# Optimization experiments

Hardware: AMD Instinct MI355X
Metric: run time of the kernel (lower is better)

Reference implementation:

```python
import jax, jax.numpy as jnp
import numpy as np

E, D, H, T = 16, 1024, 4096, 8192  # num_expert, d_model, d_hidden (4h), total tokens


def setup_inputs() -> dict:
    key = jax.random.key(0)
    k0, k1, k2, k3, k4 = jax.random.split(key, 5)
    inp = jax.random.normal(k0, (T, D), dtype=jnp.float32)
    # FMoELinear init: kaiming-uniform-like, bound = 1/sqrt(fan_in)
    s1 = 1.0 / np.sqrt(D)
    s2 = 1.0 / np.sqrt(H)
    w1 = jax.random.uniform(k1, (E, H, D), jnp.float32, -s1, s1)  # htoh4 weight [E, out, in]
    b1 = jax.random.uniform(k2, (E, H), jnp.float32, -s1, s1)
    w2 = jax.random.uniform(k3, (E, D, H), jnp.float32, -s2, s2)  # h4toh weight
    b2 = jax.random.uniform(k4, (E, D), jnp.float32, -s2, s2)
    fwd_expert_count = jnp.full((E,), T // E, dtype=jnp.int32)  # tokens per expert (sums to T)
    return dict(inp=inp, w1=w1, b1=b1, w2=w2, b2=b2, fwd_expert_count=fwd_expert_count)


def reference(inp, w1, b1, w2, b2, fwd_expert_count):
    # Grouped GEMM: tokens are sorted by expert; segment e gets expert e's FFN.
    counts = np.asarray(fwd_expert_count)          # static per-expert row counts
    offs = np.concatenate([[0], np.cumsum(counts)])
    outs = []
    for e in range(counts.shape[0]):               # loop over fixed small expert set
        seg = inp[offs[e]:offs[e + 1]]             # [n_e, D]
        h = seg @ w1[e].T + b1[e]                  # htoh4: [n_e, H]
        h = jax.nn.gelu(h, approximate=False)      # torch F.gelu default (exact)
        outs.append(h @ w2[e].T + b2[e])           # h4toh: [n_e, D]
    return jnp.concatenate(outs, axis=0)           # [T, D]
```

## Files before the change

### kernel.cpp

```cpp
#include <hip/hip_runtime.h>
#include <hip/hip_bf16.h>

typedef float f32x4 __attribute__((ext_vector_type(4)));
typedef int   i32x4 __attribute__((ext_vector_type(4)));
typedef __bf16 bf16x8 __attribute__((ext_vector_type(8)));
typedef unsigned short u16;
typedef unsigned short u16x4 __attribute__((ext_vector_type(4)));
typedef unsigned short u16x8 __attribute__((ext_vector_type(8)));

#define BM 128
#define BN 128
#define BK 32
#define NT 256
#define MAXE 32

__device__ __forceinline__ u16 f2bf(float f) {
  __bf16 h = (__bf16)f;
  return __builtin_bit_cast(u16, h);
}

__global__ __launch_bounds__(256)
void cvt_bf16(const float* __restrict__ in, u16* __restrict__ out, int n8) {
  int i = blockIdx.x * 256 + threadIdx.x;
  if (i < n8) {
    f32x4 a = *(const f32x4*)(in + (long long)i * 8);
    f32x4 b = *(const f32x4*)(in + (long long)i * 8 + 4);
    u16x8 r = { f2bf(a[0]), f2bf(a[1]), f2bf(a[2]), f2bf(a[3]),
                f2bf(b[0]), f2bf(b[1]), f2bf(b[2]), f2bf(b[3]) };
    *(u16x8*)(out + (long long)i * 8) = r;
  }
}

template<bool DO_GELU, bool OUT_BF16, int NTB>
__global__ __launch_bounds__(NT)
void ffn_gemm(const u16* __restrict__ Ain, const float* __restrict__ Bw,
              const float* __restrict__ bias, void* __restrict__ Out,
              const int* __restrict__ counts, int E, int T, int N, int K)
{
  int cs[MAXE];
#pragma unroll
  for (int j = 0; j < MAXE / 4; ++j) {
    if (j * 4 + 3 < E) {
      *(i32x4*)&cs[j * 4] = *(const i32x4*)(counts + j * 4);
    } else {
#pragma unroll
      for (int q = 0; q < 4; ++q) cs[j*4+q] = (j*4+q < E) ? counts[j*4+q] : 0;
    }
  }
  int mt = blockIdx.y, row0 = 0, e = -1, cnt = 0;
#pragma unroll
  for (int i = 0; i < MAXE; ++i) {
    if (i < E && e < 0) {
      int ntl = (cs[i] + BM - 1) / BM;
      if (mt < ntl) { e = i; cnt = cs[i]; }
      else { mt -= ntl; row0 += cs[i]; }
    }
  }
  if (e < 0) return;
  int valid = cnt - mt * BM; if (valid > BM) valid = BM;
  row0 += mt * BM;

  const float* Be = Bw + (long long)e * N * K;
  const float* be = bias + (long long)e * N;

  __shared__ u16 As[2][BM][BK];
  __shared__ u16 Bs[2][BN][BK];

  const int t = threadIdx.x;
  const int lane = t & 63;
  const int w = t >> 6, wr = w >> 1, wc = w & 1;
  const int NKT = K / BK;

  long long offA[2];
#pragma unroll
  for (int i = 0; i < 2; ++i) {
    int c = i * NT + t;
    int row = c >> 2, col = (c & 3) << 3;
    int gr = row0 + row; if (gr > T - 1) gr = T - 1;
    offA[i] = (long long)gr * K + col;
  }
  int rBrow[4], rBcol[4];
#pragma unroll
  for (int i = 0; i < 4; ++i) {
    int c = i * NT + t;
    rBrow[i] = c >> 3; rBcol[i] = (c & 7) << 2;
  }

  const int rl = lane & 15;
  const int kgf = (lane >> 4) ^ ((rl >> 1) & 3);
  const int cl = lane & 15, rg = lane >> 4;

  u16x8 rAu[2]; float rB[16];

  for (int pass = 0; pass < NTB; ++pass) {
    const int n0 = (blockIdx.x * NTB + pass) * BN;

    long long offB[4];
#pragma unroll
    for (int i = 0; i < 4; ++i)
      offB[i] = (long long)(n0 + rBrow[i]) * K + rBcol[i];

    f32x4 acc[4][4];
#pragma unroll
    for (int i = 0; i < 4; ++i)
#pragma unroll
      for (int j = 0; j < 4; ++j) acc[i][j] = (f32x4){0.f, 0.f, 0.f, 0.f};

    auto load_g = [&](int kt) {
      const int k0 = kt * BK;
#pragma unroll
      for (int i = 0; i < 2; ++i)
        rAu[i] = *(const u16x8*)(Ain + offA[i] + k0);
#pragma unroll
      for (int i = 0; i < 4; ++i) {
        f32x4 v = *(const f32x4*)(Be + offB[i] + k0);
        rB[i*4+0] = v[0]; rB[i*4+1] = v[1]; rB[i*4+2] = v[2]; rB[i*4+3] = v[3];
      }
    };

    auto store_tile = [&](int buf) {
#pragma unroll
      for (int i = 0; i < 2; ++i) {
        int c = i * NT + t;
        int row = c >> 2, col = (c & 3) << 3;
        int kg = (col >> 3) ^ ((row >> 1) & 3);
        *(u16x8*)&As[buf][row][kg * 8] = rAu[i];
      }
#pragma unroll
      for (int i = 0; i < 4; ++i) {
        int c = i * NT + t;
        int row = c >> 3, col = (c & 7) << 2;
        int kg = (col >> 3) ^ ((row >> 1) & 3);
        int off = kg * 8 + ((col >> 2) & 1) * 4;
        u16x4 pk = { f2bf(rB[i*4+0]), f2bf(rB[i*4+1]), f2bf(rB[i*4+2]), f2bf(rB[i*4+3]) };
        *(u16x4*)&Bs[buf][row][off] = pk;
      }
    };

    if (NTB > 1 && pass > 0) __syncthreads();

    load_g(0);
    store_tile(0);
    load_g(1);
    __syncthreads();

    for (int kt = 0; kt < NKT; ++kt) {
      const int cur = kt & 1;

      bf16x8 af[4], bfr[4];
#pragma unroll
      for (int mf = 0; mf < 4; ++mf)
        af[mf] = __builtin_bit_cast(bf16x8, *(const u16x8*)&As[cur][wr*64 + mf*16 + rl][kgf*8]);
#pragma unroll
      for (int nf = 0; nf < 4; ++nf)
        bfr[nf] = __builtin_bit_cast(bf16x8, *(const u16x8*)&Bs[cur][wc*64 + nf*16 + rl][kgf*8]);

      if (kt + 1 < NKT) store_tile(cur ^ 1);
      if (kt + 2 < NKT) load_g(kt + 2);

#pragma unroll
      for (int mf = 0; mf < 4; ++mf)
#pragma unroll
        for (int nf = 0; nf < 4; ++nf)
          acc[mf][nf] = __builtin_amdgcn_mfma_f32_16x16x32_bf16(af[mf], bfr[nf], acc[mf][nf], 0, 0, 0);

      if (kt + 1 < NKT) __syncthreads();
    }

#pragma unroll
    for (int mf = 0; mf < 4; ++mf) {
#pragma unroll
      for (int nf = 0; nf < 4; ++nf) {
        int gcol = n0 + wc*64 + nf*16 + cl;
        float bv = be[gcol];
#pragma unroll
        for (int r = 0; r < 4; ++r) {
          int lrow = wr*64 + mf*16 + rg*4 + r;
          if (lrow < valid) {
            float v = acc[mf][nf][r] + bv;
            if constexpr (DO_GELU)
              v = 0.5f * v * (1.0f + erff(v * 0.70710678118654752f));
            long long idx = (long long)(row0 + lrow) * N + gcol;
            if constexpr (OUT_BF16) ((u16*)Out)[idx] = f2bf(v);
            else                    ((float*)Out)[idx] = v;
          }
        }
      }
    }
  }
}

extern "C" void kernel_launch(void* const* d_in, const int* in_sizes, int n_in,
                              void* d_out, int out_size, void* d_ws, size_t ws_size,
                              hipStream_t stream) {
  const float* inp = (const float*)d_in[0];
  const float* w1  = (const float*)d_in[1];
  const float* b1  = (const float*)d_in[2];
  const float* w2  = (const float*)d_in[3];
  const float* b2  = (const float*)d_in[4];
  const int* cnts  = (const int*)d_in[5];

  const int E = in_sizes[5];
  const int H = in_sizes[2] / E;
  const int D = in_sizes[4] / E;
  const int T = in_sizes[0] / D;

  u16* hbuf = (u16*)d_ws;
  u16* ibuf = (u16*)((char*)d_ws + (size_t)T * H * 2);

  const int n8 = (T * D) / 8;
  cvt_bf16<<<dim3((n8 + 255) / 256), dim3(256), 0, stream>>>(inp, ibuf, n8);

  const int tiles = (T + BM - 1) / BM + E;

  constexpr int NTB1 = 4;
  dim3 g1(H / BN / NTB1, tiles);
  ffn_gemm<true, true, NTB1><<<g1, dim3(NT), 0, stream>>>(
      ibuf, w1, b1, (void*)hbuf, cnts, E, T, H, D);

  dim3 g2(D / BN, tiles);
  ffn_gemm<false, false, 1><<<g2, dim3(NT), 0, stream>>>(
      hbuf, w2, b2, d_out, cnts, E, T, D, H);
}
```

Before: 351.9 us.

## Use direct global-to-LDS loads with fp32 weight staging in first FFN GEMM

```diff
diff --git a/kernel.cpp b/kernel.cpp
--- a/kernel.cpp
+++ b/kernel.cpp
@@ -17,6 +17,12 @@
 __device__ __forceinline__ u16 f2bf(float f) {
   __bf16 h = (__bf16)f;
   return __builtin_bit_cast(u16, h);
+}
+
+typedef const __attribute__((address_space(1))) void GAS;
+typedef __attribute__((address_space(3))) void LAS;
+__device__ __forceinline__ void gl_lds16(const void* g, void* l) {
+  __builtin_amdgcn_global_load_lds((GAS*)g, (LAS*)l, 16, 0, 0);
 }
 
 __global__ __launch_bounds__(256)
@@ -31,34 +37,161 @@
   }
 }
 
-template<bool DO_GELU, bool OUT_BF16, int NTB>
+__device__ __forceinline__ int expert_lookup(const int* counts, int E, int bm,
+                                             int mt_in, int& row0, int& cnt, int& mt) {
+  int cs[MAXE];
+#pragma unroll
+  for (int j = 0; j < MAXE / 4; ++j) {
+    if (j * 4 + 3 < E) *(i32x4*)&cs[j * 4] = *(const i32x4*)(counts + j * 4);
+    else {
+#pragma unroll
+      for (int q = 0; q < 4; ++q) cs[j*4+q] = (j*4+q < E) ? counts[j*4+q] : 0;
+    }
+  }
+  int e = -1; row0 = 0; cnt = 0; mt = mt_in;
+#pragma unroll
+  for (int i = 0; i < MAXE; ++i) {
+    if (i < E && e < 0) {
+      int ntl = (cs[i] + bm - 1) / bm;
+      if (mt < ntl) { e = i; cnt = cs[i]; }
+      else { mt -= ntl; row0 += cs[i]; }
+    }
+  }
+  return e;
+}
+
+__global__ __launch_bounds__(NT)
+void ffn_gemm1(const u16* __restrict__ Ain, const float* __restrict__ Bw,
+               const float* __restrict__ bias, u16* __restrict__ Out,
+               const int* __restrict__ counts, int E, int T, int N, int K)
+{
+  int row0, cnt, mt;
+  int e = expert_lookup(counts, E, BM, blockIdx.y, row0, cnt, mt);
+  if (e < 0) return;
+  int valid = cnt - mt * BM; if (valid > BM) valid = BM;
+  row0 += mt * BM;
+  const int n0 = blockIdx.x * BN;
+
+  const float* Be = Bw + (long long)e * N * K;
+  const float* be = bias + (long long)e * N;
+
+  __shared__ u16  As[2][BM * BK];
+  __shared__ float Bs[2][BN * BK];
+
+  const int t = threadIdx.x;
+  const int lane = t & 63;
+  const int w = t >> 6, wr = w >> 1, wc = w & 1;
+  const int NKT = K / BK;
+
+  int aSrc[2], aDst[2];
+#pragma unroll
+  for (int s = 0; s < 2; ++s) {
+    int rb = (s * 4 + w) * 16;
+    int r = rb + (lane >> 2);
+    int gr = row0 + r; if (gr > T - 1) gr = T - 1;
+    aSrc[s] = gr * K + ((lane & 3) << 3);
+    aDst[s] = rb * BK;
+  }
+  int bSrc[4], bDst[4];
+#pragma unroll
+  for (int s = 0; s < 4; ++s) {
+    int rb = (s * 4 + w) * 8;
+    int r = rb + (lane >> 3);
+    bSrc[s] = (n0 + r) * K + (((lane & 7) ^ (r & 7)) << 2);
+    bDst[s] = rb * BK;
+  }
+
+  auto stage = [&](int buf, int kt) {
+    const int k0 = kt * BK;
+#pragma unroll
+    for (int s = 0; s < 2; ++s) gl_lds16(Ain + aSrc[s] + k0, &As[buf][aDst[s]]);
+#pragma unroll
+    for (int s = 0; s < 4; ++s) gl_lds16(Be + bSrc[s] + k0, &Bs[buf][bDst[s]]);
+  };
+
+  const int rl = lane & 15, kg = lane >> 4;
+  int aoff[4], boff[4];
+#pragma unroll
+  for (int mf = 0; mf < 4; ++mf) {
+    int R = wr * 64 + mf * 16 + rl;
+    aoff[mf] = R * BK + kg * 8;
+  }
+#pragma unroll
+  for (int nf = 0; nf < 4; ++nf) {
+    int R = wc * 64 + nf * 16 + rl;
+    int go = (2 * kg) ^ (R & 7);
+    boff[nf] = R * BK + go * 4;
+  }
+
+  f32x4 acc[4][4];
+#pragma unroll
+  for (int i = 0; i < 4; ++i)
+#pragma unroll
+    for (int j = 0; j < 4; ++j) acc[i][j] = (f32x4){0.f, 0.f, 0.f, 0.f};
+
+  stage(0, 0);
+  __syncthreads();
+
+  for (int kt = 0; kt < NKT; ++kt) {
+    const int cur = kt & 1;
+    if (kt + 1 < NKT) stage(cur ^ 1, kt + 1);
+
+    bf16x8 af[4], bfr[4];
+#pragma unroll
+    for (int mf = 0; mf < 4; ++mf)
+      af[mf] = __builtin_bit_cast(bf16x8, *(const u16x8*)&As[cur][aoff[mf]]);
+#pragma unroll
+    for (int nf = 0; nf < 4; ++nf) {
+      f32x4 lo = *(const f32x4*)&Bs[cur][boff[nf]];
+      f32x4 hi = *(const f32x4*)&Bs[cur][boff[nf] ^ 4];
+      u16x8 r = { f2bf(lo[0]), f2bf(lo[1]), f2bf(lo[2]), f2bf(lo[3]),
+                  f2bf(hi[0]), f2bf(hi[1]), f2bf(hi[2]), f2bf(hi[3]) };
+      bfr[nf] = __builtin_bit_cast(bf16x8, r);
+    }
+
+    __builtin_amdgcn_s_setprio(1);
+#pragma unroll
+    for (int mf = 0; mf < 4; ++mf)
+#pragma unroll
+      for (int nf = 0; nf < 4; ++nf)
+        acc[mf][nf] = __builtin_amdgcn_mfma_f32_16x16x32_bf16(af[mf], bfr[nf], acc[mf][nf], 0, 0, 0);
+    __builtin_amdgcn_s_setprio(0);
+
+    __syncthreads();
+  }
+
+  const int cl = lane & 15, rg = lane >> 4;
+#pragma unroll
+  for (int mf = 0; mf < 4; ++mf) {
+#pragma unroll
+    for (int nf = 0; nf < 4; ++nf) {
+      int gcol = n0 + wc * 64 + nf * 16 + cl;
+      float bv = be[gcol];
+#pragma unroll
+      for (int r = 0; r < 4; ++r) {
+        int lrow = wr * 64 + mf * 16 + rg * 4 + r;
+        if (lrow < valid) {
+          float v = acc[mf][nf][r] + bv;
+          v = 0.5f * v * (1.0f + erff(v * 0.70710678118654752f));
+          Out[(long long)(row0 + lrow) * N + gcol] = f2bf(v);
+        }
+      }
+    }
+  }
+}
+
+template<bool DO_GELU, bool OUT_BF16>
 __global__ __launch_bounds__(NT)
 void ffn_gemm(const u16* __restrict__ Ain, const float* __restrict__ Bw,
               const float* __restrict__ bias, void* __restrict__ Out,
               const int* __restrict__ counts, int E, int T, int N, int K)
 {
-  int cs[MAXE];
-#pragma unroll
-  for (int j = 0; j < MAXE / 4; ++j) {
-    if (j * 4 + 3 < E) {
-      *(i32x4*)&cs[j * 4] = *(const i32x4*)(counts + j * 4);
-    } else {
-#pragma unroll
-      for (int q = 0; q < 4; ++q) cs[j*4+q] = (j*4+q < E) ? counts[j*4+q] : 0;
-    }
-  }
-  int mt = blockIdx.y, row0 = 0, e = -1, cnt = 0;
-#pragma unroll
-  for (int i = 0; i < MAXE; ++i) {
-    if (i < E && e < 0) {
-      int ntl = (cs[i] + BM - 1) / BM;
-      if (mt < ntl) { e = i; cnt = cs[i]; }
-      else { mt -= ntl; row0 += cs[i]; }
-    }
-  }
+  int row0, cnt, mt;
+  int e = expert_lookup(counts, E, BM, blockIdx.y, row0, cnt, mt);
   if (e < 0) return;
   int valid = cnt - mt * BM; if (valid > BM) valid = BM;
   row0 += mt * BM;
+  const int n0 = blockIdx.x * BN;
 
   const float* Be = Bw + (long long)e * N * K;
   const float* be = bias + (long long)e * N;
@@ -79,111 +212,100 @@
     int gr = row0 + row; if (gr > T - 1) gr = T - 1;
     offA[i] = (long long)gr * K + col;
   }
-  int rBrow[4], rBcol[4];
+  long long offB[4];
 #pragma unroll
   for (int i = 0; i < 4; ++i) {
     int c = i * NT + t;
-    rBrow[i] = c >> 3; rBcol[i] = (c & 7) << 2;
-  }
+    offB[i] = (long long)(n0 + (c >> 3)) * K + ((c & 7) << 2);
+  }
+
+  f32x4 acc[4][4];
+#pragma unroll
+  for (int i = 0; i < 4; ++i)
+#pragma unroll
+    for (int j = 0; j < 4; ++j) acc[i][j] = (f32x4){0.f, 0.f, 0.f, 0.f};
+
+  u16x8 rAu[2]; float rB[16];
+
+  auto load_g = [&](int kt) {
+    const int k0 = kt * BK;
+#pragma unroll
+    for (int i = 0; i < 2; ++i)
+      rAu[i] = *(const u16x8*)(Ain + offA[i] + k0);
+#pragma unroll
+    for (int i = 0; i < 4; ++i) {
+      f32x4 v = *(const f32x4*)(Be + offB[i] + k0);
+      rB[i*4+0] = v[0]; rB[i*4+1] = v[1]; rB[i*4+2] = v[2]; rB[i*4+3] = v[3];
+    }
+  };
+
+  auto store_tile = [&](int buf) {
+#pragma unroll
+    for (int i = 0; i < 2; ++i) {
+      int c = i * NT + t;
+      int row = c >> 2, col = (c & 3) << 3;
+      int kg2 = (col >> 3) ^ ((row >> 1) & 3);
+      *(u16x8*)&As[buf][row][kg2 * 8] = rAu[i];
+    }
+#pragma unroll
+    for (int i = 0; i < 4; ++i) {
+      int c = i * NT + t;
+      int row = c >> 3, col = (c & 7) << 2;
+      int kg2 = (col >> 3) ^ ((row >> 1) & 3);
+      int off = kg2 * 8 + ((col >> 2) & 1) * 4;
+      u16x4 pk = { f2bf(rB[i*4+0]), f2bf(rB[i*4+1]), f2bf(rB[i*4+2]), f2bf(rB[i*4+3]) };
+      *(u16x4*)&Bs[buf][row][off] = pk;
+    }
+  };
+
+  load_g(0);
+  store_tile(0);
+  load_g(1);
+  __syncthreads();
 
   const int rl = lane & 15;
   const int kgf = (lane >> 4) ^ ((rl >> 1) & 3);
+
+  for (int kt = 0; kt < NKT; ++kt) {
+    const int cur = kt & 1;
+
+    bf16x8 af[4], bfr[4];
+#pragma unroll
+    for (int mf = 0; mf < 4; ++mf)
+      af[mf] = __builtin_bit_cast(bf16x8, *(const u16x8*)&As[cur][wr*64 + mf*16 + rl][kgf*8]);
+#pragma unroll
+    for (int nf = 0; nf < 4; ++nf)
+      bfr[nf] = __builtin_bit_cast(bf16x8, *(const u16x8*)&Bs[cur][wc*64 + nf*16 + rl][kgf*8]);
+
+    if (kt + 1 < NKT) store_tile(cur ^ 1);
+    if (kt + 2 < NKT) load_g(kt + 2);
+
+#pragma unroll
+    for (int mf = 0; mf < 4; ++mf)
+#pragma unroll
+      for (int nf = 0; nf < 4; ++nf)
+        acc[mf][nf] = __builtin_amdgcn_mfma_f32_16x16x32_bf16(af[mf], bfr[nf], acc[mf][nf], 0, 0, 0);
+
+    if (kt + 1 < NKT) __syncthreads();
+  }
+
   const int cl = lane & 15, rg = lane >> 4;
-
-  u16x8 rAu[2]; float rB[16];
-
-  for (int pass = 0; pass < NTB; ++pass) {
-    const int n0 = (blockIdx.x * NTB + pass) * BN;
-
-    long long offB[4];
-#pragma unroll
-    for (int i = 0; i < 4; ++i)
-      offB[i] = (long long)(n0 + rBrow[i]) * K + rBcol[i];
-
-    f32x4 acc[4][4];
-#pragma unroll
-    for (int i = 0; i < 4; ++i)
-#pragma unroll
-      for (int j = 0; j < 4; ++j) acc[i][j] = (f32x4){0.f, 0.f, 0.f, 0.f};
-
-    auto load_g = [&](int kt) {
-      const int k0 = kt * BK;
-#pragma unroll
-      for (int i = 0; i < 2; ++i)
-        rAu[i] = *(const u16x8*)(Ain + offA[i] + k0);
-#pragma unroll
-      for (int i = 0; i < 4; ++i) {
-        f32x4 v = *(const f32x4*)(Be + offB[i] + k0);
-        rB[i*4+0] = v[0]; rB[i*4+1] = v[1]; rB[i*4+2] = v[2]; rB[i*4+3] = v[3];
-      }
-    };
-
-    auto store_tile = [&](int buf) {
-#pragma unroll
-      for (int i = 0; i < 2; ++i) {
-        int c = i * NT + t;
-        int row = c >> 2, col = (c & 3) << 3;
-        int kg = (col >> 3) ^ ((row >> 1) & 3);
-        *(u16x8*)&As[buf][row][kg * 8] = rAu[i];
-      }
-#pragma unroll
-      for (int i = 0; i < 4; ++i) {
-        int c = i * NT + t;
-        int row = c >> 3, col = (c & 7) << 2;
-        int kg = (col >> 3) ^ ((row >> 1) & 3);
-        int off = kg * 8 + ((col >> 2) & 1) * 4;
-        u16x4 pk = { f2bf(rB[i*4+0]), f2bf(rB[i*4+1]), f2bf(rB[i*4+2]), f2bf(rB[i*4+3]) };
-        *(u16x4*)&Bs[buf][row][off] = pk;
-      }
-    };
-
-    if (NTB > 1 && pass > 0) __syncthreads();
-
-    load_g(0);
-    store_tile(0);
-    load_g(1);
-    __syncthreads();
-
-    for (int kt = 0; kt < NKT; ++kt) {
-      const int cur = kt & 1;
-
-      bf16x8 af[4], bfr[4];
-#pragma unroll
-      for (int mf = 0; mf < 4; ++mf)
-        af[mf] = __builtin_bit_cast(bf16x8, *(const u16x8*)&As[cur][wr*64 + mf*16 + rl][kgf*8]);
-#pragma unroll
-      for (int nf = 0; nf < 4; ++nf)
-        bfr[nf] = __builtin_bit_cast(bf16x8, *(const u16x8*)&Bs[cur][wc*64 + nf*16 + rl][kgf*8]);
-
-      if (kt + 1 < NKT) store_tile(cur ^ 1);
-      if (kt + 2 < NKT) load_g(kt + 2);
-
-#pragma unroll
-      for (int mf = 0; mf < 4; ++mf)
-#pragma unroll
-        for (int nf = 0; nf < 4; ++nf)
-          acc[mf][nf] = __builtin_amdgcn_mfma_f32_16x16x32_bf16(af[mf], bfr[nf], acc[mf][nf], 0, 0, 0);
-
-      if (kt + 1 < NKT) __syncthreads();
-    }
-
-#pragma unroll
-    for (int mf = 0; mf < 4; ++mf) {
-#pragma unroll
-      for (int nf = 0; nf < 4; ++nf) {
-        int gcol = n0 + wc*64 + nf*16 + cl;
-        float bv = be[gcol];
-#pragma unroll
-        for (int r = 0; r < 4; ++r) {
-          int lrow = wr*64 + mf*16 + rg*4 + r;
-          if (lrow < valid) {
-            float v = acc[mf][nf][r] + bv;
-            if constexpr (DO_GELU)
-              v = 0.5f * v * (1.0f + erff(v * 0.70710678118654752f));
-            long long idx = (long long)(row0 + lrow) * N + gcol;
-            if constexpr (OUT_BF16) ((u16*)Out)[idx] = f2bf(v);
-            else                    ((float*)Out)[idx] = v;
-          }
+#pragma unroll
+  for (int mf = 0; mf < 4; ++mf) {
+#pragma unroll
+    for (int nf = 0; nf < 4; ++nf) {
+      int gcol = n0 + wc*64 + nf*16 + cl;
+      float bv = be[gcol];
+#pragma unroll
+      for (int r = 0; r < 4; ++r) {
+        int lrow = wr*64 + mf*16 + rg*4 + r;
+        if (lrow < valid) {
+          float v = acc[mf][nf][r] + bv;
+          if constexpr (DO_GELU)
+            v = 0.5f * v * (1.0f + erff(v * 0.70710678118654752f));
+          long long idx = (long long)(row0 + lrow) * N + gcol;
+          if constexpr (OUT_BF16) ((u16*)Out)[idx] = f2bf(v);
+          else                    ((float*)Out)[idx] = v;
         }
       }
     }
@@ -211,14 +333,12 @@
   const int n8 = (T * D) / 8;
   cvt_bf16<<<dim3((n8 + 255) / 256), dim3(256), 0, stream>>>(inp, ibuf, n8);
 
-  const int tiles = (T + BM - 1) / BM + E;
-
-  constexpr int NTB1 = 4;
-  dim3 g1(H / BN / NTB1, tiles);
-  ffn_gemm<true, true, NTB1><<<g1, dim3(NT), 0, stream>>>(
-      ibuf, w1, b1, (void*)hbuf, cnts, E, T, H, D);
+  const int tiles = T / BM + E;
+
+  dim3 g1(H / BN, tiles);
+  ffn_gemm1<<<g1, dim3(NT), 0, stream>>>(ibuf, w1, b1, hbuf, cnts, E, T, H, D);
 
   dim3 g2(D / BN, tiles);
-  ffn_gemm<false, false, 1><<<g2, dim3(NT), 0, stream>>>(
+  ffn_gemm<false, false><<<g2, dim3(NT), 0, stream>>>(
       hbuf, w2, b2, d_out, cnts, E, T, D, H);
 }
```

After: 346.0 us. About the same (-1.7%).

## Split GELU into separate elementwise pass and drop multi-pass N tiling

Applied to the files above, without the earlier changes.

```diff
diff --git a/kernel.cpp b/kernel.cpp
--- a/kernel.cpp
+++ b/kernel.cpp
@@ -17,6 +17,10 @@
 __device__ __forceinline__ u16 f2bf(float f) {
   __bf16 h = (__bf16)f;
   return __builtin_bit_cast(u16, h);
+}
+__device__ __forceinline__ float bf2f(u16 u) {
+  unsigned v = (unsigned)u << 16;
+  return __builtin_bit_cast(float, v);
 }
 
 __global__ __launch_bounds__(256)
@@ -31,34 +35,57 @@
   }
 }
 
-template<bool DO_GELU, bool OUT_BF16, int NTB>
+__global__ __launch_bounds__(256)
+void gelu_pass(u16* __restrict__ h, int n8) {
+  int i = blockIdx.x * 256 + threadIdx.x;
+  if (i < n8) {
+    u16x8 v = *(const u16x8*)(h + (long long)i * 8);
+    u16x8 r;
+#pragma unroll
+    for (int j = 0; j < 8; ++j) {
+      float x = bf2f(v[j]);
+      x = 0.5f * x * (1.0f + erff(x * 0.70710678118654752f));
+      r[j] = f2bf(x);
+    }
+    *(u16x8*)(h + (long long)i * 8) = r;
+  }
+}
+
+__device__ __forceinline__ int expert_lookup(const int* counts, int E, int bm,
+                                             int mt_in, int& row0, int& cnt, int& mt) {
+  int cs[MAXE];
+#pragma unroll
+  for (int j = 0; j < MAXE / 4; ++j) {
+    if (j * 4 + 3 < E) *(i32x4*)&cs[j * 4] = *(const i32x4*)(counts + j * 4);
+    else {
+#pragma unroll
+      for (int q = 0; q < 4; ++q) cs[j*4+q] = (j*4+q < E) ? counts[j*4+q] : 0;
+    }
+  }
+  int e = -1; row0 = 0; cnt = 0; mt = mt_in;
+#pragma unroll
+  for (int i = 0; i < MAXE; ++i) {
+    if (i < E && e < 0) {
+      int ntl = (cs[i] + bm - 1) / bm;
+      if (mt < ntl) { e = i; cnt = cs[i]; }
+      else { mt -= ntl; row0 += cs[i]; }
+    }
+  }
+  return e;
+}
+
+template<bool OUT_BF16>
 __global__ __launch_bounds__(NT)
 void ffn_gemm(const u16* __restrict__ Ain, const float* __restrict__ Bw,
               const float* __restrict__ bias, void* __restrict__ Out,
               const int* __restrict__ counts, int E, int T, int N, int K)
 {
-  int cs[MAXE];
-#pragma unroll
-  for (int j = 0; j < MAXE / 4; ++j) {
-    if (j * 4 + 3 < E) {
-      *(i32x4*)&cs[j * 4] = *(const i32x4*)(counts + j * 4);
-    } else {
-#pragma unroll
-      for (int q = 0; q < 4; ++q) cs[j*4+q] = (j*4+q < E) ? counts[j*4+q] : 0;
-    }
-  }
-  int mt = blockIdx.y, row0 = 0, e = -1, cnt = 0;
-#pragma unroll
-  for (int i = 0; i < MAXE; ++i) {
-    if (i < E && e < 0) {
-      int ntl = (cs[i] + BM - 1) / BM;
-      if (mt < ntl) { e = i; cnt = cs[i]; }
-      else { mt -= ntl; row0 += cs[i]; }
-    }
-  }
+  int row0, cnt, mt;
+  int e = expert_lookup(counts, E, BM, blockIdx.y, row0, cnt, mt);
   if (e < 0) return;
   int valid = cnt - mt * BM; if (valid > BM) valid = BM;
   row0 += mt * BM;
+  const int n0 = blockIdx.x * BN;
 
   const float* Be = Bw + (long long)e * N * K;
   const float* be = bias + (long long)e * N;
@@ -79,111 +106,98 @@
     int gr = row0 + row; if (gr > T - 1) gr = T - 1;
     offA[i] = (long long)gr * K + col;
   }
-  int rBrow[4], rBcol[4];
+  long long offB[4];
 #pragma unroll
   for (int i = 0; i < 4; ++i) {
     int c = i * NT + t;
-    rBrow[i] = c >> 3; rBcol[i] = (c & 7) << 2;
-  }
+    offB[i] = (long long)(n0 + (c >> 3)) * K + ((c & 7) << 2);
+  }
+
+  f32x4 acc[4][4];
+#pragma unroll
+  for (int i = 0; i < 4; ++i)
+#pragma unroll
+    for (int j = 0; j < 4; ++j) acc[i][j] = (f32x4){0.f, 0.f, 0.f, 0.f};
+
+  u16x8 rAu[2]; float rB[16];
+
+  auto load_g = [&](int kt) {
+    const int k0 = kt * BK;
+#pragma unroll
+    for (int i = 0; i < 2; ++i)
+      rAu[i] = *(const u16x8*)(Ain + offA[i] + k0);
+#pragma unroll
+    for (int i = 0; i < 4; ++i) {
+      f32x4 v = *(const f32x4*)(Be + offB[i] + k0);
+      rB[i*4+0] = v[0]; rB[i*4+1] = v[1]; rB[i*4+2] = v[2]; rB[i*4+3] = v[3];
+    }
+  };
+
+  auto store_tile = [&](int buf) {
+#pragma unroll
+    for (int i = 0; i < 2; ++i) {
+      int c = i * NT + t;
+      int row = c >> 2, col = (c & 3) << 3;
+      int kg2 = (col >> 3) ^ ((row >> 1) & 3);
+      *(u16x8*)&As[buf][row][kg2 * 8] = rAu[i];
+    }
+#pragma unroll
+    for (int i = 0; i < 4; ++i) {
+      int c = i * NT + t;
+      int row = c >> 3, col = (c & 7) << 2;
+      int kg2 = (col >> 3) ^ ((row >> 1) & 3);
+      int off = kg2 * 8 + ((col >> 2) & 1) * 4;
+      u16x4 pk = { f2bf(rB[i*4+0]), f2bf(rB[i*4+1]), f2bf(rB[i*4+2]), f2bf(rB[i*4+3]) };
+      *(u16x4*)&Bs[buf][row][off] = pk;
+    }
+  };
+
+  load_g(0);
+  store_tile(0);
+  load_g(1);
+  __syncthreads();
 
   const int rl = lane & 15;
   const int kgf = (lane >> 4) ^ ((rl >> 1) & 3);
+
+  for (int kt = 0; kt < NKT; ++kt) {
+    const int cur = kt & 1;
+
+    bf16x8 af[4], bfr[4];
+#pragma unroll
+    for (int mf = 0; mf < 4; ++mf)
+      af[mf] = __builtin_bit_cast(bf16x8, *(const u16x8*)&As[cur][wr*64 + mf*16 + rl][kgf*8]);
+#pragma unroll
+    for (int nf = 0; nf < 4; ++nf)
+      bfr[nf] = __builtin_bit_cast(bf16x8, *(const u16x8*)&Bs[cur][wc*64 + nf*16 + rl][kgf*8]);
+
+    if (kt + 1 < NKT) store_tile(cur ^ 1);
+    if (kt + 2 < NKT) load_g(kt + 2);
+
+#pragma unroll
+    for (int mf = 0; mf < 4; ++mf)
+#pragma unroll
+      for (int nf = 0; nf < 4; ++nf)
+        acc[mf][nf] = __builtin_amdgcn_mfma_f32_16x16x32_bf16(af[mf], bfr[nf], acc[mf][nf], 0, 0, 0);
+
+    if (kt + 1 < NKT) __syncthreads();
+  }
+
   const int cl = lane & 15, rg = lane >> 4;
-
-  u16x8 rAu[2]; float rB[16];
-
-  for (int pass = 0; pass < NTB; ++pass) {
-    const int n0 = (blockIdx.x * NTB + pass) * BN;
-
-    long long offB[4];
-#pragma unroll
-    for (int i = 0; i < 4; ++i)
-      offB[i] = (long long)(n0 + rBrow[i]) * K + rBcol[i];
-
-    f32x4 acc[4][4];
-#pragma unroll
-    for (int i = 0; i < 4; ++i)
-#pragma unroll
-      for (int j = 0; j < 4; ++j) acc[i][j] = (f32x4){0.f, 0.f, 0.f, 0.f};
-
-    auto load_g = [&](int kt) {
-      const int k0 = kt * BK;
-#pragma unroll
-      for (int i = 0; i < 2; ++i)
-        rAu[i] = *(const u16x8*)(Ain + offA[i] + k0);
-#pragma unroll
-      for (int i = 0; i < 4; ++i) {
-        f32x4 v = *(const f32x4*)(Be + offB[i] + k0);
-        rB[i*4+0] = v[0]; rB[i*4+1] = v[1]; rB[i*4+2] = v[2]; rB[i*4+3] = v[3];
-      }
-    };
-
-    auto store_tile = [&](int buf) {
-#pragma unroll
-      for (int i = 0; i < 2; ++i) {
-        int c = i * NT + t;
-        int row = c >> 2, col = (c & 3) << 3;
-        int kg = (col >> 3) ^ ((row >> 1) & 3);
-        *(u16x8*)&As[buf][row][kg * 8] = rAu[i];
-      }
-#pragma unroll
-      for (int i = 0; i < 4; ++i) {
-        int c = i * NT + t;
-        int row = c >> 3, col = (c & 7) << 2;
-        int kg = (col >> 3) ^ ((row >> 1) & 3);
-        int off = kg * 8 + ((col >> 2) & 1) * 4;
-        u16x4 pk = { f2bf(rB[i*4+0]), f2bf(rB[i*4+1]), f2bf(rB[i*4+2]), f2bf(rB[i*4+3]) };
-        *(u16x4*)&Bs[buf][row][off] = pk;
-      }
-    };
-
-    if (NTB > 1 && pass > 0) __syncthreads();
-
-    load_g(0);
-    store_tile(0);
-    load_g(1);
-    __syncthreads();
-
-    for (int kt = 0; kt < NKT; ++kt) {
-      const int cur = kt & 1;
-
-      bf16x8 af[4], bfr[4];
-#pragma unroll
-      for (int mf = 0; mf < 4; ++mf)
-        af[mf] = __builtin_bit_cast(bf16x8, *(const u16x8*)&As[cur][wr*64 + mf*16 + rl][kgf*8]);
-#pragma unroll
-      for (int nf = 0; nf < 4; ++nf)
-        bfr[nf] = __builtin_bit_cast(bf16x8, *(const u16x8*)&Bs[cur][wc*64 + nf*16 + rl][kgf*8]);
-
-      if (kt + 1 < NKT) store_tile(cur ^ 1);
-      if (kt + 2 < NKT) load_g(kt + 2);
-
-#pragma unroll
-      for (int mf = 0; mf < 4; ++mf)
-#pragma unroll
-        for (int nf = 0; nf < 4; ++nf)
-          acc[mf][nf] = __builtin_amdgcn_mfma_f32_16x16x32_bf16(af[mf], bfr[nf], acc[mf][nf], 0, 0, 0);
-
-      if (kt + 1 < NKT) __syncthreads();
-    }
-
-#pragma unroll
-    for (int mf = 0; mf < 4; ++mf) {
-#pragma unroll
-      for (int nf = 0; nf < 4; ++nf) {
-        int gcol = n0 + wc*64 + nf*16 + cl;
-        float bv = be[gcol];
-#pragma unroll
-        for (int r = 0; r < 4; ++r) {
-          int lrow = wr*64 + mf*16 + rg*4 + r;
-          if (lrow < valid) {
-            float v = acc[mf][nf][r] + bv;
-            if constexpr (DO_GELU)
-              v = 0.5f * v * (1.0f + erff(v * 0.70710678118654752f));
-            long long idx = (long long)(row0 + lrow) * N + gcol;
-            if constexpr (OUT_BF16) ((u16*)Out)[idx] = f2bf(v);
-            else                    ((float*)Out)[idx] = v;
-          }
+#pragma unroll
+  for (int mf = 0; mf < 4; ++mf) {
+#pragma unroll
+    for (int nf = 0; nf < 4; ++nf) {
+      int gcol = n0 + wc*64 + nf*16 + cl;
+      float bv = be[gcol];
+#pragma unroll
+      for (int r = 0; r < 4; ++r) {
+        int lrow = wr*64 + mf*16 + rg*4 + r;
+        if (lrow < valid) {
+          float v = acc[mf][nf][r] + bv;
+          long long idx = (long long)(row0 + lrow) * N + gcol;
+          if constexpr (OUT_BF16) ((u16*)Out)[idx] = f2bf(v);
+          else                    ((float*)Out)[idx] = v;
         }
       }
     }
@@ -208,17 +222,17 @@
   u16* hbuf = (u16*)d_ws;
   u16* ibuf = (u16*)((char*)d_ws + (size_t)T * H * 2);
 
-  const int n8 = (T * D) / 8;
-  cvt_bf16<<<dim3((n8 + 255) / 256), dim3(256), 0, stream>>>(inp, ibuf, n8);
-
-  const int tiles = (T + BM - 1) / BM + E;
-
-  constexpr int NTB1 = 4;
-  dim3 g1(H / BN / NTB1, tiles);
-  ffn_gemm<true, true, NTB1><<<g1, dim3(NT), 0, stream>>>(
-      ibuf, w1, b1, (void*)hbuf, cnts, E, T, H, D);
-
-  dim3 g2(D / BN, tiles);
-  ffn_gemm<false, false, 1><<<g2, dim3(NT), 0, stream>>>(
+  const int n8i = (T * D) / 8;
+  cvt_bf16<<<dim3((n8i + 255) / 256), dim3(256), 0, stream>>>(inp, ibuf, n8i);
+
+  const int tiles = T / BM + E;
+
+  ffn_gemm<true><<<dim3(H / BN, tiles), dim3(NT), 0, stream>>>(
+      ibuf, w1, b1, hbuf, cnts, E, T, H, D);
+
+  const int n8h = (T * H) / 8;
+  gelu_pass<<<dim3((n8h + 255) / 256), dim3(256), 0, stream>>>(hbuf, n8h);
+
+  ffn_gemm<false><<<dim3(D / BN, tiles), dim3(NT), 0, stream>>>(
       hbuf, w2, b2, d_out, cnts, E, T, D, H);
 }
```

New measurement: 345.1 us. About the same (-1.9%).
